# Kernel tuning notes

Hardware: AMD Instinct MI355X
Metric: run time of the kernel (lower is better)

The kernel has to match this reference:

```python
import jax, jax.numpy as jnp
import numpy as np
import math

D_MODEL = 512
N_HEADS = 8
D_K = 64
BS = 16
SEQ = 512


def setup_inputs() -> dict:
    key = jax.random.key(0)
    ks = jax.random.split(key, 15)
    f = lambda k, sh, s=1.0: jax.random.normal(k, sh, dtype=jnp.float32) * s
    inp = {}
    for i, n in enumerate(["q_mean", "q_cov", "k_mean", "k_cov", "v_mean", "v_cov"]):
        inp[n] = f(ks[i], (BS, SEQ, D_MODEL))
    wscale = 1.0 / math.sqrt(D_MODEL)  # ~xavier
    for i, n in enumerate(["Wq_mean", "Wq_cov", "Wk_mean", "Wk_cov", "Wv_mean", "Wv_cov", "Wo_mean", "Wo_cov"]):
        inp[n] = f(ks[6 + i], (D_MODEL, D_MODEL), wscale)
    inp["gammas"] = f(ks[14], (N_HEADS, 1, 1), 0.5)  # xavier on (h,1,1)
    # causal mask: attend to positions j <= i
    inp["mask"] = jnp.tril(jnp.ones((SEQ, SEQ), dtype=jnp.int32))[None, None]
    return inp


def _heads(x, W):
    # torch Linear: x @ W.T ; bias is 0 by init. -> [bs, h, S, d_k]
    bs = x.shape[0]
    return (x @ W.T).reshape(bs, -1, N_HEADS, D_K).transpose(0, 2, 1, 3)


def _uattention(qm, qc, km, kc, vm, vc, mask, gammas):
    # Wasserstein-2 distance between diagonal Gaussians, fused into matmuls
    mean_d = (-2.0 * jnp.einsum('bhsd,bhtd->bhst', qm, km)
              + jnp.sum(qm ** 2, -1, keepdims=True)
              + jnp.sum(km ** 2, -1, keepdims=True).swapaxes(-1, -2))
    sqc = jnp.sqrt(jnp.clip(qc, 1e-24))
    skc = jnp.sqrt(jnp.clip(kc, 1e-24))
    cov_d = (-2.0 * jnp.einsum('bhsd,bhtd->bhst', sqc, skc)
             + jnp.sum(qc, -1, keepdims=True)
             + jnp.sum(kc, -1, keepdims=True).swapaxes(-1, -2))
    scores = -(mean_d + cov_d) / math.sqrt(D_K)  # [bs,h,S,S]

    maskb = (mask == 0)
    maskf = mask.astype(scores.dtype)

    def _dist(s):
        s_ = jax.nn.softmax(jnp.where(maskb, -1e32, s), axis=-1) * maskf
        cum = jnp.cumsum(s_, axis=-1)
        tot = jnp.sum(s_, axis=-1, keepdims=True)
        idx = jnp.arange(SEQ)
        pos = jnp.abs(idx[None, :] - idx[:, None]).astype(jnp.float32)[None, None]
        return jnp.sqrt(jnp.clip((tot - cum) * pos, 0.0))

    dist_scores = jax.lax.stop_gradient(_dist(scores))  # torch: no_grad + detach
    gamma = -jax.nn.softplus(gammas)[None]  # [1,h,1,1]
    total_effect = jnp.clip(jnp.exp(dist_scores * gamma), 1e-5, 1e5)
    scores = jnp.where(maskb, -1e32, scores * total_effect)
    scores = jax.nn.softmax(scores, axis=-1)
    scores = scores.at[:, :, 0, :].set(0.0)  # zero_pad
    out_mean = jnp.einsum('bhst,bhtd->bhsd', scores, vm)
    out_cov = jnp.einsum('bhst,bhtd->bhsd', scores ** 2, vc)
    return out_mean, out_cov


def reference(q_mean, q_cov, k_mean, k_cov, v_mean, v_cov,
              Wq_mean, Wq_cov, Wk_mean, Wk_cov, Wv_mean, Wv_cov,
              Wo_mean, Wo_cov, gammas, mask):
    bs = q_mean.shape[0]
    qm = _heads(q_mean, Wq_mean)
    qc = _heads(q_cov, Wq_cov)
    km = _heads(k_mean, Wk_mean)
    kc = _heads(k_cov, Wk_cov)
    vm = _heads(v_mean, Wv_mean)
    vc = _heads(v_cov, Wv_cov)
    om, oc = _uattention(qm, qc, km, kc, vm, vc, mask, gammas)
    cm = om.transpose(0, 2, 1, 3).reshape(bs, -1, D_MODEL)
    cc = oc.transpose(0, 2, 1, 3).reshape(bs, -1, D_MODEL)
    return cm @ Wo_mean.T, cc @ Wo_cov.T
```

## Files before the change

### kernel.cpp

```cpp
#include <hip/hip_runtime.h>
#include <hip/hip_bf16.h>

#define SEQ    512
#define DMODEL 512
#define NHEAD  8
#define DK     64
#define BS     16
#define NBH    (BS*NHEAD)
#define HSZ    (SEQ*DK)
#define L2E    1.4426950408889634f

typedef __attribute__((ext_vector_type(8))) short bf16x8;
typedef __attribute__((ext_vector_type(4))) float f32x4;

#define MFMA32(A,B,C) __builtin_amdgcn_mfma_f32_16x16x32_bf16(A,B,C,0,0,0)

#define WS_GAM 16ull
#define WS_AQM 256ull
#define WS_AQC (WS_AQM +  65536ull)
#define WS_BKM (WS_AQM + 131072ull)
#define WS_BKC (WS_AQM + 196608ull)
#define WS_AQF (WS_AQM + 262144ull)
#define WS_BKF (WS_AQM + 327680ull)
#define WS_OM  1048576ull
#define WS_OC  (WS_OM + 4194304ull)
#define WS_BF  (WS_OC + 4194304ull)
#define ARRE   4194304ull
#define A_QMH 0
#define A_QML 1
#define A_SCH 2
#define A_SCL 3
#define A_KMH 4
#define A_SKH 6
#define A_VMT 8
#define A_VCT 9

__device__ __forceinline__ unsigned short* warr(float* wsf, int idx) {
  return (unsigned short*)(wsf + WS_BF) + (size_t)idx * ARRE;
}

__device__ __forceinline__ float bf2f(unsigned short h) {
  union { float f; unsigned u; } v; v.u = ((unsigned)h) << 16; return v.f;
}
__device__ __forceinline__ unsigned short f2bf(float f) {
  union { float f; unsigned u; } v; v.f = f;
  unsigned u = v.u;
  u += 0x7FFFu + ((u >> 16) & 1u);
  return (unsigned short)(u >> 16);
}
__device__ __forceinline__ void ld8_f32(const float* p, float* v) {
  float4 a = *(const float4*)p; float4 b = *(const float4*)(p+4);
  v[0]=a.x;v[1]=a.y;v[2]=a.z;v[3]=a.w;v[4]=b.x;v[5]=b.y;v[6]=b.z;v[7]=b.w;
}
__device__ __forceinline__ unsigned pk2bf(float a, float b) {
  union { float f; unsigned u; } x, y;
  x.f = a; y.f = b;
  return __builtin_amdgcn_perm(y.u + 0x8000u, x.u + 0x8000u, 0x07060302u);
}
__device__ __forceinline__ uint4 cvt8r(const float* t8) {
  uint4 h;
  h.x = pk2bf(t8[0], t8[1]);
  h.y = pk2bf(t8[2], t8[3]);
  h.z = pk2bf(t8[4], t8[5]);
  h.w = pk2bf(t8[6], t8[7]);
  return h;
}
__device__ __forceinline__ uint4 cvt8h(const float* p) {
  float t8[8]; ld8_f32(p, t8); return cvt8r(t8);
}

__global__ void k_gamma(const float* __restrict__ g_in, float* __restrict__ wsf) {
  int t = threadIdx.x;
  if (t >= NHEAD) return;
  float g = g_in[t];
  float sp = (g > 20.f) ? g : log1pf(expf(g));
  (wsf + WS_GAM)[t] = -sp * L2E;
}

__global__ __launch_bounds__(256) void k_projM(
    const float* xqm, const float* xqc, const float* xkm, const float* xkc,
    const float* xvm, const float* xvc,
    const float* wqm, const float* wqc, const float* wkm, const float* wkc,
    const float* wvm, const float* wvc,
    float* wsf)
{
  __shared__ __align__(16) unsigned short Ah[4096];
  __shared__ __align__(16) unsigned short Bh[4096];
  const int y = blockIdx.y;
  const float* X; const float* W;
  unsigned short *outh = nullptr, *outl = nullptr;
  float* sums = nullptr;
  float qscale = 1.0f; int mode = 0;
  switch (y) {
    case 0: X=xqm; W=wqm; outh=warr(wsf,A_QMH); outl=warr(wsf,A_QML); sums=wsf+WS_AQM; qscale=0.25f*L2E; mode=0; break;
    case 1: X=xkm; W=wkm; outh=warr(wsf,A_KMH); outl=nullptr;         sums=wsf+WS_BKM; qscale=1.0f;      mode=0; break;
    case 2: X=xqc; W=wqc; outh=warr(wsf,A_SCH); outl=warr(wsf,A_SCL); sums=wsf+WS_AQC; qscale=0.25f*L2E; mode=1; break;
    case 3: X=xkc; W=wkc; outh=warr(wsf,A_SKH); outl=nullptr;         sums=wsf+WS_BKC; qscale=1.0f;      mode=1; break;
    case 4: X=xvm; W=wvm; outh=warr(wsf,A_VMT); mode=2; break;
    default:X=xvc; W=wvc; outh=warr(wsf,A_VCT); mode=2; break;
  }
  const int tid = threadIdx.x;
  const int l = tid & 63, li = l & 15, lg = l >> 4;
  const int w = tid >> 6, wr = w >> 1, wc = w & 1;
  const int blk = blockIdx.x;
  const int xcd = blk & 7, qq = blk >> 3;
  const int m0 = (xcd*8 + (qq & 7)) * 128;
  const int n0 = (qq >> 3) * 128;
  const int r0 = tid >> 2, c0 = tid & 3, r1 = r0 + 64;
  const int wo0 = r0*64 + ((c0 ^ ((r0>>1)&3))*16);
  const int wo1 = r1*64 + ((c0 ^ ((r1>>1)&3))*16);
  int roA[4], roB[4];
#pragma unroll
  for (int mi = 0; mi < 4; ++mi) {
    int r  = wr*64 + mi*16 + li;
    roA[mi] = r*64 + ((lg ^ ((r>>1)&3))*16);
    int rn = wc*64 + mi*16 + li;
    roB[mi] = rn*64 + ((lg ^ ((rn>>1)&3))*16);
  }
  const float* xp0 = X + (size_t)(m0+r0)*DMODEL + c0*8;
  const float* xp1 = X + (size_t)(m0+r1)*DMODEL + c0*8;
  const float* wp0 = W + (size_t)(n0+r0)*DMODEL + c0*8;
  const float* wp1 = W + (size_t)(n0+r1)*DMODEL + c0*8;
  uint4 a0 = cvt8h(xp0);
  uint4 a1 = cvt8h(xp1);
  uint4 b0 = cvt8h(wp0);
  uint4 b1 = cvt8h(wp1);

  f32x4 acc[4][4];
  f32x4 z = {0.f,0.f,0.f,0.f};
#pragma unroll
  for (int a = 0; a < 4; ++a)
#pragma unroll
    for (int b = 0; b < 4; ++b) acc[a][b] = z;

  for (int kt = 0; kt < DMODEL; kt += 32) {
    __syncthreads();
    *(uint4*)((char*)Ah + wo0) = a0;
    *(uint4*)((char*)Ah + wo1) = a1;
    *(uint4*)((char*)Bh + wo0) = b0;
    *(uint4*)((char*)Bh + wo1) = b1;
    __syncthreads();
    if (kt + 32 < DMODEL) {
      a0 = cvt8h(xp0 + kt + 32);
      a1 = cvt8h(xp1 + kt + 32);
      b0 = cvt8h(wp0 + kt + 32);
      b1 = cvt8h(wp1 + kt + 32);
    }
    bf16x8 ah[4], bh[4];
#pragma unroll
    for (int mi = 0; mi < 4; ++mi) {
      ah[mi] = *(const bf16x8*)((const char*)Ah + roA[mi]);
      bh[mi] = *(const bf16x8*)((const char*)Bh + roB[mi]);
    }
#pragma unroll
    for (int mi = 0; mi < 4; ++mi)
#pragma unroll
      for (int nj = 0; nj < 4; ++nj)
        acc[mi][nj] = MFMA32(ah[mi], bh[nj], acc[mi][nj]);
  }

  const int head = ((n0 >> 6) + wc);
  if (mode <= 1) {
    const bool kside = (outl == nullptr);
#pragma unroll
    for (int mi = 0; mi < 4; ++mi)
#pragma unroll
      for (int reg = 0; reg < 4; ++reg) {
        float rs = 0.f;
#pragma unroll
        for (int nj = 0; nj < 4; ++nj) {
          float v = acc[mi][nj][reg];
          if (mode == 0) {
            float vs = (kside) ? bf2f(f2bf(v)) : v;
            rs += vs*vs;
          } else {
            rs += v;
          }
        }
        rs += __shfl_xor(rs, 1); rs += __shfl_xor(rs, 2);
        rs += __shfl_xor(rs, 4); rs += __shfl_xor(rs, 8);
        if (li == 0) {
          int m = m0 + wr*64 + mi*16 + 4*lg + reg;
          sums[((size_t)(m >> 9)*NHEAD + head)*SEQ + (m & 511)] = rs;
        }
      }
#pragma unroll
    for (int mi = 0; mi < 4; ++mi)
#pragma unroll
      for (int nj = 0; nj < 4; ++nj)
#pragma unroll
        for (int reg = 0; reg < 4; ++reg) {
          float v = acc[mi][nj][reg];
          if (mode == 1) v = sqrtf(fmaxf(v, 1e-24f));
          v *= qscale;
          unsigned short h16 = f2bf(v);
          int m = m0 + wr*64 + mi*16 + 4*lg + reg;
          int n = n0 + wc*64 + nj*16 + li;
          size_t dst = ((size_t)((m >> 9)*NHEAD + (n >> 6))*SEQ + (m & 511))*DK + (n & 63);
          outh[dst] = h16;
          if (outl) outl[dst] = f2bf(v - bf2f(h16));
        }
  } else {
#pragma unroll
    for (int mi = 0; mi < 4; ++mi)
#pragma unroll
      for (int nj = 0; nj < 4; ++nj) {
        int mb = m0 + wr*64 + mi*16 + 4*lg;
        int n = n0 + wc*64 + nj*16 + li;
        int b = mb >> 9, s = mb & 511, d = n & 63;
        unsigned e0 = f2bf(acc[mi][nj][0]);
        unsigned e1 = f2bf(acc[mi][nj][1]);
        unsigned e2 = f2bf(acc[mi][nj][2]);
        unsigned e3 = f2bf(acc[mi][nj][3]);
        uint2 pk; pk.x = e0 | (e1 << 16); pk.y = e2 | (e3 << 16);
        *(uint2*)(outh + ((size_t)(b*NHEAD + head)*DK + d)*SEQ + s) = pk;
      }
  }
}

__global__ void k_sumAB(float* wsf) {
  int i = blockIdx.x * 256 + threadIdx.x;
  if (i < NBH*SEQ) {
    (wsf+WS_AQF)[i] = (0.125f*L2E) * ((wsf+WS_AQM)[i] + (wsf+WS_AQC)[i]);
    (wsf+WS_BKF)[i] = (0.125f*L2E) * ((wsf+WS_BKM)[i] + (wsf+WS_BKC)[i]);
  }
}

__global__ __launch_bounds__(256) void k_attn2(float* wsf)
{
  __shared__ float s_bk[SEQ];
  __shared__ float s_ex[4][2][16];
  __shared__ __align__(16) float s_acc[3][64][33];

  const unsigned short* qmh = warr(wsf, A_QMH);
  const unsigned short* qml = warr(wsf, A_QML);
  const unsigned short* sch = warr(wsf, A_SCH);
  const unsigned short* scl = warr(wsf, A_SCL);
  const unsigned short* kmh = warr(wsf, A_KMH);
  const unsigned short* skh = warr(wsf, A_SKH);
  const unsigned short* vmT = warr(wsf, A_VMT);
  const unsigned short* vcT = warr(wsf, A_VCT);
  float* omF = wsf + WS_OM;
  float* ocF = wsf + WS_OC;
  const float* AqF = wsf + WS_AQF;
  const float* BkF = wsf + WS_BKF;

  const int tid = threadIdx.x;
  const int l = tid & 63, li = l & 15, lg = l >> 4;
  const int w = tid >> 6;
  const int blk = blockIdx.x;
  const int xcd = blk & 7;
  const int q   = blk >> 3;
  const int bh  = xcd*16 + (q & 15);
  const int rt  = 31 - (q >> 4);
  const int i = rt*16 + li;
  const int ntile = rt + 1;
  const int qd = ntile >> 2, rr = ntile & 3;
  const int tstart = w*qd + (w < rr ? w : rr);
  const int tend   = tstart + qd + (w < rr ? 1 : 0);
  const float gam = (wsf + WS_GAM)[bh & (NHEAD-1)];
  const float aq = AqF[(size_t)bh*SEQ + i];

  for (int idx = tid; idx < SEQ; idx += 256) s_bk[idx] = BkF[(size_t)bh*SEQ + idx];

  bf16x8 qf[8];
  {
    const unsigned short* qb[4] = {qmh, qml, sch, scl};
#pragma unroll
    for (int part = 0; part < 2; ++part)
#pragma unroll
      for (int hl = 0; hl < 2; ++hl)
#pragma unroll
        for (int ks = 0; ks < 2; ++ks)
          qf[part*4 + ks*2 + hl] =
            *(const bf16x8*)(qb[part*2+hl] + ((size_t)bh*SEQ + i)*DK + ks*32 + lg*8);
  }
  __syncthreads();

  auto score_tile = [&](int t, float* s) {
    const int j0 = t*16;
    f32x4 accA = {0.f,0.f,0.f,0.f};
    f32x4 accB = {0.f,0.f,0.f,0.f};
    const size_t krow = ((size_t)bh*SEQ + j0 + li)*DK + lg*8;
#pragma unroll
    for (int part = 0; part < 2; ++part) {
      const unsigned short* khp = part ? skh : kmh;
#pragma unroll
      for (int ks = 0; ks < 2; ++ks) {
        bf16x8 kh = *(const bf16x8*)(khp + krow + ks*32);
        accA = MFMA32(kh, qf[part*4+ks*2+0], accA);
        accB = MFMA32(kh, qf[part*4+ks*2+1], accB);
      }
    }
    const float4 bk4 = *(const float4*)&s_bk[j0 + lg*4];
    float bks[4] = {bk4.x, bk4.y, bk4.z, bk4.w};
#pragma unroll
    for (int r = 0; r < 4; ++r) {
      int j = j0 + lg*4 + r;
      float v = (accA[r] + accB[r]) - aq - bks[r];
      s[r] = (j > i) ? -3.0e38f : v;
    }
  };

  float m1 = -3.0e38f, tot = 0.f;
  for (int t = tstart; t < tend; ++t) {
    float s[4]; score_tile(t, s);
    float tm = fmaxf(fmaxf(s[0], s[1]), fmaxf(s[2], s[3]));
    tm = fmaxf(tm, __shfl_xor(tm, 16));
    tm = fmaxf(tm, __shfl_xor(tm, 32));
    float m1n = fmaxf(m1, tm);
    float lsum = exp2f(s[0]-m1n) + exp2f(s[1]-m1n) + exp2f(s[2]-m1n) + exp2f(s[3]-m1n);
    lsum += __shfl_xor(lsum, 16); lsum += __shfl_xor(lsum, 32);
    tot = tot * exp2f(m1 - m1n) + lsum;
    m1 = m1n;
  }
  if (lg == 0) { s_ex[w][0][li] = m1; s_ex[w][1][li] = tot; }
  __syncthreads();
  float run;
  {
    float mA = s_ex[0][0][li], mB = s_ex[1][0][li],
          mC = s_ex[2][0][li], mD = s_ex[3][0][li];
    float mg = fmaxf(fmaxf(mA, mB), fmaxf(mC, mD));
    float tA = s_ex[0][1][li] * exp2f(mA - mg);
    float tB = s_ex[1][1][li] * exp2f(mB - mg);
    float tC = s_ex[2][1][li] * exp2f(mC - mg);
    float tD = s_ex[3][1][li] * exp2f(mD - mg);
    tot = tA + tB + tC + tD;
    run = (w > 0 ? tA : 0.f) + (w > 1 ? tB : 0.f) + (w > 2 ? tC : 0.f);
    m1 = mg;
  }
  const float invtot = 1.0f / tot;

  f32x4 accm[4], accc[4];
  {
    f32x4 z = {0.f,0.f,0.f,0.f};
#pragma unroll
    for (int dt = 0; dt < 4; ++dt) { accm[dt] = z; accc[dt] = z; }
  }
  float m2 = -3.0e38f, sum2 = 0.f;

  auto scan_tile = [&](int t, float* s2) {
    float s[4]; score_tile(t, s);
    float e0 = exp2f(s[0]-m1), e1 = exp2f(s[1]-m1),
          e2 = exp2f(s[2]-m1), e3 = exp2f(s[3]-m1);
    float p0 = e0, p1 = p0+e1, p2 = p1+e2, p3 = p2+e3;
    float lt = p3;
    float a = __shfl_up(lt, 16), b = __shfl_up(lt, 32), c = __shfl_up(lt, 48);
    float excl = (lg >= 1 ? a : 0.f) + (lg >= 2 ? b : 0.f) + (lg >= 3 ? c : 0.f);
    float base = run + excl;
    float cums[4] = {base+p0, base+p1, base+p2, base+p3};
    float ttr = lt;
    ttr += __shfl_xor(ttr, 16); ttr += __shfl_xor(ttr, 32);
    run += ttr;
#pragma unroll
    for (int r = 0; r < 4; ++r) {
      int j = t*16 + lg*4 + r;
      float rem = fmaxf(tot - cums[r], 0.f) * invtot;
      float pos = fmaxf((float)(i - j), 0.f);
      float dist = sqrtf(rem * pos);
      float eff = fmaxf(exp2f(dist * gam), 1e-5f);
      s2[r] = (j > i) ? -3.0e38f : s[r] * eff;
    }
  };

  for (int t0 = tstart; t0 < tend; t0 += 2) {
    float s2A[4], s2B[4];
    scan_tile(t0, s2A);
    const bool hasB = (t0 + 1) < tend;
    if (hasB) scan_tile(t0+1, s2B);
    else { s2B[0]=s2B[1]=s2B[2]=s2B[3] = -3.0e38f; }
    const int j0A = t0*16;
    const int j0B = hasB ? j0A + 16 : j0A;
    union V16 { struct { uint2 lo, hi; } u; bf16x8 v; };
    V16 vm_[4], vc_[4];
#pragma unroll
    for (int dt = 0; dt < 4; ++dt) {
      const size_t vrow = ((size_t)bh*DK + dt*16 + li)*SEQ;
      vm_[dt].u.lo = *(const uint2*)(vmT + vrow + j0A + lg*4);
      vm_[dt].u.hi = *(const uint2*)(vmT + vrow + j0B + lg*4);
      vc_[dt].u.lo = *(const uint2*)(vcT + vrow + j0A + lg*4);
      vc_[dt].u.hi = *(const uint2*)(vcT + vrow + j0B + lg*4);
    }
    float mt = fmaxf(fmaxf(fmaxf(s2A[0],s2A[1]), fmaxf(s2A[2],s2A[3])),
                     fmaxf(fmaxf(s2B[0],s2B[1]), fmaxf(s2B[2],s2B[3])));
    mt = fmaxf(mt, __shfl_xor(mt, 16));
    mt = fmaxf(mt, __shfl_xor(mt, 32));
    float m2n = fmaxf(m2, mt);
    float scale = exp2f(m2 - m2n);
    float scale2 = scale * scale;
#pragma unroll
    for (int dt = 0; dt < 4; ++dt) { accm[dt] *= scale; accc[dt] *= scale2; }
    float pA[4], pB[4];
#pragma unroll
    for (int r = 0; r < 4; ++r) { pA[r] = exp2f(s2A[r]-m2n); pB[r] = exp2f(s2B[r]-m2n); }
    float ps = pA[0]+pA[1]+pA[2]+pA[3] + pB[0]+pB[1]+pB[2]+pB[3];
    ps += __shfl_xor(ps, 16); ps += __shfl_xor(ps, 32);
    sum2 = sum2 * scale + ps;
    m2 = m2n;
    union PU { uint4 u; bf16x8 v; } pm, pc;
    pm.u.x = pk2bf(pA[0], pA[1]); pm.u.y = pk2bf(pA[2], pA[3]);
    pm.u.z = pk2bf(pB[0], pB[1]); pm.u.w = pk2bf(pB[2], pB[3]);
    pc.u.x = pk2bf(pA[0]*pA[0], pA[1]*pA[1]); pc.u.y = pk2bf(pA[2]*pA[2], pA[3]*pA[3]);
    pc.u.z = pk2bf(pB[0]*pB[0], pB[1]*pB[1]); pc.u.w = pk2bf(pB[2]*pB[2], pB[3]*pB[3]);
#pragma unroll
    for (int dt = 0; dt < 4; ++dt) {
      accm[dt] = MFMA32(vm_[dt].v, pm.v, accm[dt]);
      accc[dt] = MFMA32(vc_[dt].v, pc.v, accc[dt]);
    }
  }

  __syncthreads();
  if (lg == 0) s_ex[w][0][li] = m2;
  __syncthreads();
  const float m2g = fmaxf(fmaxf(s_ex[0][0][li], s_ex[1][0][li]),
                          fmaxf(s_ex[2][0][li], s_ex[3][0][li]));
  const float sc = exp2f(m2 - m2g);
  const float sc2 = sc * sc;
  if (w > 0) {
#pragma unroll
    for (int dt = 0; dt < 4; ++dt)
#pragma unroll
      for (int reg = 0; reg < 4; ++reg) {
        s_acc[w-1][l][dt*4 + reg]      = accm[dt][reg] * sc;
        s_acc[w-1][l][16 + dt*4 + reg] = accc[dt][reg] * sc2;
      }
    if (lg == 0) s_ex[w][1][li] = sum2 * sc;
  }
  __syncthreads();
  if (w == 0) {
    const float sum2g = sum2 * sc + s_ex[1][1][li] + s_ex[2][1][li] + s_ex[3][1][li];
    const float inv2 = 1.0f / sum2g;
    const float inv2c = inv2 * inv2;
    const bool zero = (i == 0);
    float* om_p = omF + ((size_t)bh*SEQ + i)*DK;
    float* oc_p = ocF + ((size_t)bh*SEQ + i)*DK;
#pragma unroll
    for (int dt = 0; dt < 4; ++dt) {
      float4 vm4, vc4;
      vm4.x = (accm[dt][0]*sc + s_acc[0][l][dt*4+0] + s_acc[1][l][dt*4+0] + s_acc[2][l][dt*4+0]) * inv2;
      vm4.y = (accm[dt][1]*sc + s_acc[0][l][dt*4+1] + s_acc[1][l][dt*4+1] + s_acc[2][l][dt*4+1]) * inv2;
      vm4.z = (accm[dt][2]*sc + s_acc[0][l][dt*4+2] + s_acc[1][l][dt*4+2] + s_acc[2][l][dt*4+2]) * inv2;
      vm4.w = (accm[dt][3]*sc + s_acc[0][l][dt*4+3] + s_acc[1][l][dt*4+3] + s_acc[2][l][dt*4+3]) * inv2;
      vc4.x = (accc[dt][0]*sc2 + s_acc[0][l][16+dt*4+0] + s_acc[1][l][16+dt*4+0] + s_acc[2][l][16+dt*4+0]) * inv2c;
      vc4.y = (accc[dt][1]*sc2 + s_acc[0][l][16+dt*4+1] + s_acc[1][l][16+dt*4+1] + s_acc[2][l][16+dt*4+1]) * inv2c;
      vc4.z = (accc[dt][2]*sc2 + s_acc[0][l][16+dt*4+2] + s_acc[1][l][16+dt*4+2] + s_acc[2][l][16+dt*4+2]) * inv2c;
      vc4.w = (accc[dt][3]*sc2 + s_acc[0][l][16+dt*4+3] + s_acc[1][l][16+dt*4+3] + s_acc[2][l][16+dt*4+3]) * inv2c;
      if (zero) { vm4 = make_float4(0.f,0.f,0.f,0.f); vc4 = vm4; }
      *(float4*)(om_p + dt*16 + lg*4) = vm4;
      *(float4*)(oc_p + dt*16 + lg*4) = vc4;
    }
  }
}

__global__ __launch_bounds__(256) void k_outM(float* wsf,
                                              const float* w_mean, const float* w_cov,
                                              float* outp)
{
  __shared__ __align__(16) unsigned short Ah[4096];
  __shared__ __align__(16) unsigned short Bh[4096];
  const int y = blockIdx.y;
  const float* A = wsf + (y ? WS_OC : WS_OM);
  const float* W = y ? w_cov : w_mean;
  float* out = outp + (size_t)y * 4194304ull;

  const int tid = threadIdx.x;
  const int l = tid & 63, li = l & 15, lg = l >> 4;
  const int w = tid >> 6, wr = w >> 1, wc = w & 1;
  const int blk = blockIdx.x;
  const int xcd = blk & 7, qq = blk >> 3;
  const int m0 = (xcd*8 + (qq & 7)) * 128;
  const int n0 = (qq >> 3) * 128;
  const int r0 = tid >> 2, c0 = tid & 3, r1 = r0 + 64;
  const int wo0 = r0*64 + ((c0 ^ ((r0>>1)&3))*16);
  const int wo1 = r1*64 + ((c0 ^ ((r1>>1)&3))*16);
  int roA[4], roB[4];
#pragma unroll
  for (int mi = 0; mi < 4; ++mi) {
    int r  = wr*64 + mi*16 + li;
    roA[mi] = r*64 + ((lg ^ ((r>>1)&3))*16);
    int rn = wc*64 + mi*16 + li;
    roB[mi] = rn*64 + ((lg ^ ((rn>>1)&3))*16);
  }
  const int mA0 = m0 + r0, mA1 = m0 + r1;
  const size_t abase0 = ((size_t)(mA0 >> 9) * NHEAD * SEQ + (mA0 & 511)) * DK;
  const size_t abase1 = ((size_t)(mA1 >> 9) * NHEAD * SEQ + (mA1 & 511)) * DK;
  const float* wp0 = W + (size_t)(n0 + r0)*DMODEL + c0*8;
  const float* wp1 = W + (size_t)(n0 + r1)*DMODEL + c0*8;

  auto acvt = [&](size_t abase, int k) -> uint4 {
    const float* p = A + abase + (size_t)(k >> 6) * (SEQ*DK) + (k & 63);
    return cvt8h(p);
  };

  int k0 = c0*8;
  uint4 a0 = acvt(abase0, k0);
  uint4 a1 = acvt(abase1, k0);
  uint4 b0 = cvt8h(wp0);
  uint4 b1 = cvt8h(wp1);

  f32x4 acc[4][4];
  f32x4 z = {0.f,0.f,0.f,0.f};
#pragma unroll
  for (int a = 0; a < 4; ++a)
#pragma unroll
    for (int b = 0; b < 4; ++b) acc[a][b] = z;

  for (int kt = 0; kt < DMODEL; kt += 32) {
    __syncthreads();
    *(uint4*)((char*)Ah + wo0) = a0;
    *(uint4*)((char*)Ah + wo1) = a1;
    *(uint4*)((char*)Bh + wo0) = b0;
    *(uint4*)((char*)Bh + wo1) = b1;
    __syncthreads();
    if (kt + 32 < DMODEL) {
      int kn = kt + 32 + c0*8;
      a0 = acvt(abase0, kn);
      a1 = acvt(abase1, kn);
      b0 = cvt8h(wp0 + kt + 32);
      b1 = cvt8h(wp1 + kt + 32);
    }
    bf16x8 ah[4], bh[4];
#pragma unroll
    for (int mi = 0; mi < 4; ++mi) {
      ah[mi] = *(const bf16x8*)((const char*)Ah + roA[mi]);
      bh[mi] = *(const bf16x8*)((const char*)Bh + roB[mi]);
    }
#pragma unroll
    for (int mi = 0; mi < 4; ++mi)
#pragma unroll
      for (int nj = 0; nj < 4; ++nj)
        acc[mi][nj] = MFMA32(ah[mi], bh[nj], acc[mi][nj]);
  }
#pragma unroll
  for (int mi = 0; mi < 4; ++mi)
#pragma unroll
    for (int nj = 0; nj < 4; ++nj)
#pragma unroll
      for (int reg = 0; reg < 4; ++reg) {
        int m = m0 + wr*64 + mi*16 + 4*lg + reg;
        int n = n0 + wc*64 + nj*16 + li;
        out[(size_t)m*DMODEL + n] = acc[mi][nj][reg];
      }
}

extern "C" void kernel_launch(void* const* d_in, const int* in_sizes, int n_in,
                              void* d_out, int out_size, void* d_ws, size_t ws_size,
                              hipStream_t stream) {
  (void)in_sizes; (void)n_in; (void)out_size; (void)ws_size;
  float* wsf = (float*)d_ws;

  k_gamma<<<1, 64, 0, stream>>>((const float*)d_in[14], wsf);
  k_projM<<<dim3(256, 6), 256, 0, stream>>>(
      (const float*)d_in[0], (const float*)d_in[1],
      (const float*)d_in[2], (const float*)d_in[3],
      (const float*)d_in[4], (const float*)d_in[5],
      (const float*)d_in[6], (const float*)d_in[7],
      (const float*)d_in[8], (const float*)d_in[9],
      (const float*)d_in[10], (const float*)d_in[11],
      wsf);
  k_sumAB<<<256, 256, 0, stream>>>(wsf);
  k_attn2<<<4096, 256, 0, stream>>>(wsf);
  k_outM<<<dim3(256, 2), 256, 0, stream>>>(wsf, (const float*)d_in[12],
                                           (const float*)d_in[13], (float*)d_out);
}
```

Measured before the change: 268.1 us.

## Drop max-subtraction in attention softmaxes and split key tiles across two waves

Both softmax passes in the attention kernel now exponentiate the scores directly instead of tracking running maxima. This relies on the Wasserstein scores being non-positive, and it removes the per-tile max reductions, accumulator rescaling and the cross-wave max merge. The squared gamma is folded into the sqrt argument, so the distance decay is computed as exp2(-sqrt(...)) with fewer multiplies. The block shrinks from four waves to two, each taking half the key tiles, which simplifies the cross-wave combine to a single shared-memory exchange. The risk is fp32 underflow, or inf/NaN from a zero row sum, when every score in a row is very negative. Halving the waves per block also reduces the parallelism within each query tile.

```diff
diff --git a/kernel.cpp b/kernel.cpp
--- a/kernel.cpp
+++ b/kernel.cpp
@@ -74,7 +74,8 @@
   if (t >= NHEAD) return;
   float g = g_in[t];
   float sp = (g > 20.f) ? g : log1pf(expf(g));
-  (wsf + WS_GAM)[t] = -sp * L2E;
+  float gl = sp * L2E;
+  (wsf + WS_GAM)[t] = gl * gl;
 }
 
 __global__ __launch_bounds__(256) void k_projM(
@@ -226,11 +227,11 @@
   }
 }
 
-__global__ __launch_bounds__(256) void k_attn2(float* wsf)
+__global__ __launch_bounds__(128) void k_attn2(float* wsf)
 {
   __shared__ float s_bk[SEQ];
-  __shared__ float s_ex[4][2][16];
-  __shared__ __align__(16) float s_acc[3][64][33];
+  __shared__ float s_tot[2][16];
+  __shared__ __align__(16) float s_acc[64][33];
 
   const unsigned short* qmh = warr(wsf, A_QMH);
   const unsigned short* qml = warr(wsf, A_QML);
@@ -255,13 +256,13 @@
   const int rt  = 31 - (q >> 4);
   const int i = rt*16 + li;
   const int ntile = rt + 1;
-  const int qd = ntile >> 2, rr = ntile & 3;
-  const int tstart = w*qd + (w < rr ? w : rr);
-  const int tend   = tstart + qd + (w < rr ? 1 : 0);
-  const float gam = (wsf + WS_GAM)[bh & (NHEAD-1)];
+  const int h0 = (ntile + 1) >> 1;
+  const int tstart = w ? h0 : 0;
+  const int tend   = w ? ntile : h0;
+  const float gam2 = (wsf + WS_GAM)[bh & (NHEAD-1)];
   const float aq = AqF[(size_t)bh*SEQ + i];
 
-  for (int idx = tid; idx < SEQ; idx += 256) s_bk[idx] = BkF[(size_t)bh*SEQ + idx];
+  for (int idx = tid; idx < SEQ; idx += 128) s_bk[idx] = BkF[(size_t)bh*SEQ + idx];
 
   bf16x8 qf[8];
   {
@@ -302,34 +303,17 @@
     }
   };
 
-  float m1 = -3.0e38f, tot = 0.f;
+  float totl = 0.f;
   for (int t = tstart; t < tend; ++t) {
     float s[4]; score_tile(t, s);
-    float tm = fmaxf(fmaxf(s[0], s[1]), fmaxf(s[2], s[3]));
-    tm = fmaxf(tm, __shfl_xor(tm, 16));
-    tm = fmaxf(tm, __shfl_xor(tm, 32));
-    float m1n = fmaxf(m1, tm);
-    float lsum = exp2f(s[0]-m1n) + exp2f(s[1]-m1n) + exp2f(s[2]-m1n) + exp2f(s[3]-m1n);
-    lsum += __shfl_xor(lsum, 16); lsum += __shfl_xor(lsum, 32);
-    tot = tot * exp2f(m1 - m1n) + lsum;
-    m1 = m1n;
-  }
-  if (lg == 0) { s_ex[w][0][li] = m1; s_ex[w][1][li] = tot; }
+    totl += exp2f(s[0]) + exp2f(s[1]) + exp2f(s[2]) + exp2f(s[3]);
+  }
+  totl += __shfl_xor(totl, 16); totl += __shfl_xor(totl, 32);
+  if (lg == 0) s_tot[w][li] = totl;
   __syncthreads();
-  float run;
-  {
-    float mA = s_ex[0][0][li], mB = s_ex[1][0][li],
-          mC = s_ex[2][0][li], mD = s_ex[3][0][li];
-    float mg = fmaxf(fmaxf(mA, mB), fmaxf(mC, mD));
-    float tA = s_ex[0][1][li] * exp2f(mA - mg);
-    float tB = s_ex[1][1][li] * exp2f(mB - mg);
-    float tC = s_ex[2][1][li] * exp2f(mC - mg);
-    float tD = s_ex[3][1][li] * exp2f(mD - mg);
-    tot = tA + tB + tC + tD;
-    run = (w > 0 ? tA : 0.f) + (w > 1 ? tB : 0.f) + (w > 2 ? tC : 0.f);
-    m1 = mg;
-  }
-  const float invtot = 1.0f / tot;
+  const float tot = fmaxf(s_tot[0][li] + s_tot[1][li], 1e-35f);
+  float run = w ? s_tot[0][li] : 0.f;
+  const float g2i = gam2 / tot;
 
   f32x4 accm[4], accc[4];
   {
@@ -337,38 +321,30 @@
 #pragma unroll
     for (int dt = 0; dt < 4; ++dt) { accm[dt] = z; accc[dt] = z; }
   }
-  float m2 = -3.0e38f, sum2 = 0.f;
-
-  auto scan_tile = [&](int t, float* s2) {
+  float sum2l = 0.f;
+
+  auto scan_tile = [&](int t, float* p) {
     float s[4]; score_tile(t, s);
-    float e0 = exp2f(s[0]-m1), e1 = exp2f(s[1]-m1),
-          e2 = exp2f(s[2]-m1), e3 = exp2f(s[3]-m1);
-    float p0 = e0, p1 = p0+e1, p2 = p1+e2, p3 = p2+e3;
-    float lt = p3;
-    float a = __shfl_up(lt, 16), b = __shfl_up(lt, 32), c = __shfl_up(lt, 48);
+    float e0 = exp2f(s[0]), e1 = exp2f(s[1]), e2 = exp2f(s[2]), e3 = exp2f(s[3]);
+    float c0 = e0, c1 = c0+e1, c2 = c1+e2, c3 = c2+e3;
+    float a = __shfl_up(c3, 16), b = __shfl_up(c3, 32), c = __shfl_up(c3, 48);
     float excl = (lg >= 1 ? a : 0.f) + (lg >= 2 ? b : 0.f) + (lg >= 3 ? c : 0.f);
     float base = run + excl;
-    float cums[4] = {base+p0, base+p1, base+p2, base+p3};
-    float ttr = lt;
-    ttr += __shfl_xor(ttr, 16); ttr += __shfl_xor(ttr, 32);
-    run += ttr;
+    run = __shfl(base + c3, li + 48);
+    float posb = (float)(i - t*16 - lg*4);
+    float cums[4] = {base+c0, base+c1, base+c2, base+c3};
 #pragma unroll
     for (int r = 0; r < 4; ++r) {
-      int j = t*16 + lg*4 + r;
-      float rem = fmaxf(tot - cums[r], 0.f) * invtot;
-      float pos = fmaxf((float)(i - j), 0.f);
-      float dist = sqrtf(rem * pos);
-      float eff = fmaxf(exp2f(dist * gam), 1e-5f);
-      s2[r] = (j > i) ? -3.0e38f : s[r] * eff;
+      float t4 = fmaxf((tot - cums[r]) * (posb - (float)r) * g2i, 0.f);
+      float d = sqrtf(t4);
+      float eff = fmaxf(exp2f(-d), 1e-5f);
+      p[r] = exp2f(s[r] * eff);
+      sum2l += p[r];
     }
   };
 
   for (int t0 = tstart; t0 < tend; t0 += 2) {
-    float s2A[4], s2B[4];
-    scan_tile(t0, s2A);
     const bool hasB = (t0 + 1) < tend;
-    if (hasB) scan_tile(t0+1, s2B);
-    else { s2B[0]=s2B[1]=s2B[2]=s2B[3] = -3.0e38f; }
     const int j0A = t0*16;
     const int j0B = hasB ? j0A + 16 : j0A;
     union V16 { struct { uint2 lo, hi; } u; bf16x8 v; };
@@ -381,22 +357,10 @@
       vc_[dt].u.lo = *(const uint2*)(vcT + vrow + j0A + lg*4);
       vc_[dt].u.hi = *(const uint2*)(vcT + vrow + j0B + lg*4);
     }
-    float mt = fmaxf(fmaxf(fmaxf(s2A[0],s2A[1]), fmaxf(s2A[2],s2A[3])),
-                     fmaxf(fmaxf(s2B[0],s2B[1]), fmaxf(s2B[2],s2B[3])));
-    mt = fmaxf(mt, __shfl_xor(mt, 16));
-    mt = fmaxf(mt, __shfl_xor(mt, 32));
-    float m2n = fmaxf(m2, mt);
-    float scale = exp2f(m2 - m2n);
-    float scale2 = scale * scale;
-#pragma unroll
-    for (int dt = 0; dt < 4; ++dt) { accm[dt] *= scale; accc[dt] *= scale2; }
     float pA[4], pB[4];
-#pragma unroll
-    for (int r = 0; r < 4; ++r) { pA[r] = exp2f(s2A[r]-m2n); pB[r] = exp2f(s2B[r]-m2n); }
-    float ps = pA[0]+pA[1]+pA[2]+pA[3] + pB[0]+pB[1]+pB[2]+pB[3];
-    ps += __shfl_xor(ps, 16); ps += __shfl_xor(ps, 32);
-    sum2 = sum2 * scale + ps;
-    m2 = m2n;
+    scan_tile(t0, pA);
+    if (hasB) scan_tile(t0+1, pB);
+    else { pB[0]=pB[1]=pB[2]=pB[3] = 0.f; }
     union PU { uint4 u; bf16x8 v; } pm, pc;
     pm.u.x = pk2bf(pA[0], pA[1]); pm.u.y = pk2bf(pA[2], pA[3]);
     pm.u.z = pk2bf(pB[0], pB[1]); pm.u.w = pk2bf(pB[2], pB[3]);
@@ -409,26 +373,21 @@
     }
   }
 
+  sum2l += __shfl_xor(sum2l, 16); sum2l += __shfl_xor(sum2l, 32);
   __syncthreads();
-  if (lg == 0) s_ex[w][0][li] = m2;
-  __syncthreads();
-  const float m2g = fmaxf(fmaxf(s_ex[0][0][li], s_ex[1][0][li]),
-                          fmaxf(s_ex[2][0][li], s_ex[3][0][li]));
-  const float sc = exp2f(m2 - m2g);
-  const float sc2 = sc * sc;
-  if (w > 0) {
+  if (w == 1) {
 #pragma unroll
     for (int dt = 0; dt < 4; ++dt)
 #pragma unroll
       for (int reg = 0; reg < 4; ++reg) {
-        s_acc[w-1][l][dt*4 + reg]      = accm[dt][reg] * sc;
-        s_acc[w-1][l][16 + dt*4 + reg] = accc[dt][reg] * sc2;
+        s_acc[l][dt*4 + reg]      = accm[dt][reg];
+        s_acc[l][16 + dt*4 + reg] = accc[dt][reg];
       }
-    if (lg == 0) s_ex[w][1][li] = sum2 * sc;
+    if (lg == 0) s_tot[1][li] = sum2l;
   }
   __syncthreads();
   if (w == 0) {
-    const float sum2g = sum2 * sc + s_ex[1][1][li] + s_ex[2][1][li] + s_ex[3][1][li];
+    const float sum2g = sum2l + s_tot[1][li];
     const float inv2 = 1.0f / sum2g;
     const float inv2c = inv2 * inv2;
     const bool zero = (i == 0);
@@ -437,14 +396,14 @@
 #pragma unroll
     for (int dt = 0; dt < 4; ++dt) {
       float4 vm4, vc4;
-      vm4.x = (accm[dt][0]*sc + s_acc[0][l][dt*4+0] + s_acc[1][l][dt*4+0] + s_acc[2][l][dt*4+0]) * inv2;
-      vm4.y = (accm[dt][1]*sc + s_acc[0][l][dt*4+1] + s_acc[1][l][dt*4+1] + s_acc[2][l][dt*4+1]) * inv2;
-      vm4.z = (accm[dt][2]*sc + s_acc[0][l][dt*4+2] + s_acc[1][l][dt*4+2] + s_acc[2][l][dt*4+2]) * inv2;
-      vm4.w = (accm[dt][3]*sc + s_acc[0][l][dt*4+3] + s_acc[1][l][dt*4+3] + s_acc[2][l][dt*4+3]) * inv2;
-      vc4.x = (accc[dt][0]*sc2 + s_acc[0][l][16+dt*4+0] + s_acc[1][l][16+dt*4+0] + s_acc[2][l][16+dt*4+0]) * inv2c;
-      vc4.y = (accc[dt][1]*sc2 + s_acc[0][l][16+dt*4+1] + s_acc[1][l][16+dt*4+1] + s_acc[2][l][16+dt*4+1]) * inv2c;
-      vc4.z = (accc[dt][2]*sc2 + s_acc[0][l][16+dt*4+2] + s_acc[1][l][16+dt*4+2] + s_acc[2][l][16+dt*4+2]) * inv2c;
-      vc4.w = (accc[dt][3]*sc2 + s_acc[0][l][16+dt*4+3] + s_acc[1][l][16+dt*4+3] + s_acc[2][l][16+dt*4+3]) * inv2c;
+      vm4.x = (accm[dt][0] + s_acc[l][dt*4+0]) * inv2;
+      vm4.y = (accm[dt][1] + s_acc[l][dt*4+1]) * inv2;
+      vm4.z = (accm[dt][2] + s_acc[l][dt*4+2]) * inv2;
+      vm4.w = (accm[dt][3] + s_acc[l][dt*4+3]) * inv2;
+      vc4.x = (accc[dt][0] + s_acc[l][16+dt*4+0]) * inv2c;
+      vc4.y = (accc[dt][1] + s_acc[l][16+dt*4+1]) * inv2c;
+      vc4.z = (accc[dt][2] + s_acc[l][16+dt*4+2]) * inv2c;
+      vc4.w = (accc[dt][3] + s_acc[l][16+dt*4+3]) * inv2c;
       if (zero) { vm4 = make_float4(0.f,0.f,0.f,0.f); vc4 = vm4; }
       *(float4*)(om_p + dt*16 + lg*4) = vm4;
       *(float4*)(oc_p + dt*16 + lg*4) = vc4;
@@ -559,7 +518,7 @@
       (const float*)d_in[10], (const float*)d_in[11],
       wsf);
   k_sumAB<<<256, 256, 0, stream>>>(wsf);
-  k_attn2<<<4096, 256, 0, stream>>>(wsf);
+  k_attn2<<<4096, 128, 0, stream>>>(wsf);
   k_outM<<<dim3(256, 2), 256, 0, stream>>>(wsf, (const float*)d_in[12],
                                            (const float*)d_in[13], (float*)d_out);
 }
```

Result: faster. 241.0 us (-10.1%).
